# Kernel optimization log

Measured on AMD Instinct MI355X. Metric: run time of the kernel, lower is better.

The kernel has to match this reference:

```python
import jax, jax.numpy as jnp
import numpy as np

N_NODES = 50000
N_EDGES = 640000
IN_DIM = 128
HID_DIM = 128


def setup_inputs() -> dict:
    key = jax.random.key(0)
    k1, k2, k3 = jax.random.split(key, 3)
    x = jax.random.normal(k1, (N_NODES, IN_DIM), dtype=jnp.float32)
    edge_index = jax.random.randint(k2, (2, N_EDGES), 0, N_NODES, dtype=jnp.int64)
    # GCNConv linear weight (glorot-ish scale) and bias
    W = jax.random.normal(k3, (IN_DIM, HID_DIM), dtype=jnp.float32) * (1.0 / np.sqrt(IN_DIM))
    b = jnp.zeros((HID_DIM,), dtype=jnp.float32)
    return {"x": x, "edge_index": edge_index, "W": W, "b": b}


def reference(x, edge_index, W, b):
    # PyG GCNConv: add self-loops, symmetric normalization deg^{-1/2} A deg^{-1/2},
    # linear transform, scatter-add aggregation, bias; then ReLU (SimpleGCN).
    N = x.shape[0]
    loops = jnp.arange(N, dtype=edge_index.dtype)
    src = jnp.concatenate([edge_index[0], loops])  # [E+N]
    dst = jnp.concatenate([edge_index[1], loops])  # [E+N]

    # degree of destination nodes (including self-loops)
    ones = jnp.ones(src.shape[0], dtype=x.dtype)
    deg = jax.ops.segment_sum(ones, dst, num_segments=N)  # [N]
    dinv = jnp.where(deg > 0, jax.lax.rsqrt(deg), 0.0)
    norm = dinv[src] * dinv[dst]  # [E+N]

    h = x @ W  # [N, H] dense GEMM first (PyG transforms before propagate)
    msg = h[src] * norm[:, None]  # gather + scale, [E+N, H]
    agg = jax.ops.segment_sum(msg, dst, num_segments=N)  # scatter-add, [N, H]
    return jax.nn.relu(agg + b)
```

## Files before the change

### kernel.cpp

```cpp
#include <hip/hip_runtime.h>
#include <cstdint>

#define NN 50000
#define NE 640000
#define DIM 128
#define CAP 64
#define CSTRIDE 16
#define GEMM_TILES ((NN + 63) / 64)
#define FILL_BLOCKS (NE / 256)
#define GATHER_BLOCKS (NN * 16 / 256)

typedef __attribute__((ext_vector_type(8))) short bf16x8;
typedef __attribute__((ext_vector_type(8))) unsigned short u16x8;
typedef __attribute__((ext_vector_type(4))) float f32x4;

static __device__ __forceinline__ short f2bf(float f) {
    union { float f; uint32_t u; } v; v.f = f;
    uint32_t r = v.u + 0x7FFFu + ((v.u >> 16) & 1u);
    return (short)(r >> 16);
}
static __device__ __forceinline__ float bf2f(unsigned short u) {
    union { uint32_t u; float f; } v; v.u = ((uint32_t)u) << 16;
    return v.f;
}

__global__ __launch_bounds__(256) void k_gemm(const float* __restrict__ x,
                                              const float* __restrict__ W,
                                              unsigned short* __restrict__ h_bf,
                                              int4* __restrict__ cntp4) {
    __shared__ bf16x8 Bs[2048];
    const int tid = threadIdx.x;
    const int gid = blockIdx.x * 256 + tid;
    for (int i = gid; i < NN * CSTRIDE / 4; i += GEMM_TILES * 256)
        cntp4[i] = make_int4(0, 0, 0, 0);

    #pragma unroll
    for (int i = 0; i < 8; ++i) {
        const int t = tid + i * 256;
        const int n = t >> 8;
        const int kk = (t >> 6) & 3;
        const int l = t & 63;
        const int c = n * 16 + (l & 15);
        const int k0 = kk * 32 + (l >> 4) * 8;
        bf16x8 v;
        #pragma unroll
        for (int j = 0; j < 8; ++j) v[j] = f2bf(W[(k0 + j) * DIM + c]);
        Bs[t] = v;
    }

    const int wave = tid >> 6;
    const int lane = tid & 63;
    const int rbase = blockIdx.x * 64 + wave * 16;
    const int rA = rbase + (lane & 15);
    const int kg = lane >> 4;

    bf16x8 a[4];
    if (rA < NN) {
        const float* xr = x + (size_t)rA * DIM + kg * 8;
        #pragma unroll
        for (int kk = 0; kk < 4; ++kk) {
            const float4 f0 = *reinterpret_cast<const float4*>(xr + kk * 32);
            const float4 f1 = *reinterpret_cast<const float4*>(xr + kk * 32 + 4);
            a[kk][0] = f2bf(f0.x); a[kk][1] = f2bf(f0.y);
            a[kk][2] = f2bf(f0.z); a[kk][3] = f2bf(f0.w);
            a[kk][4] = f2bf(f1.x); a[kk][5] = f2bf(f1.y);
            a[kk][6] = f2bf(f1.z); a[kk][7] = f2bf(f1.w);
        }
    } else {
        #pragma unroll
        for (int kk = 0; kk < 4; ++kk) a[kk] = (bf16x8)0;
    }
    __syncthreads();

    const int rC0 = rbase + (lane >> 4) * 4;
    const int col = lane & 15;
    #pragma unroll
    for (int n = 0; n < 8; ++n) {
        f32x4 acc = {0.f, 0.f, 0.f, 0.f};
        #pragma unroll
        for (int kk = 0; kk < 4; ++kk) {
            const bf16x8 b = Bs[(n * 4 + kk) * 64 + lane];
            acc = __builtin_amdgcn_mfma_f32_16x16x32_bf16(a[kk], b, acc, 0, 0, 0);
        }
        #pragma unroll
        for (int i = 0; i < 4; ++i) {
            const int r = rC0 + i;
            if (r < NN)
                h_bf[(size_t)r * DIM + n * 16 + col] = (unsigned short)f2bf(acc[i]);
        }
    }
}

__global__ __launch_bounds__(256) void k_fill(const int* __restrict__ src,
                                              const int* __restrict__ dst,
                                              int* __restrict__ cntp,
                                              int* __restrict__ srt) {
    const int i = blockIdx.x * 256 + threadIdx.x;
    const int s = src[i];
    const int d = dst[i];
    const int pos = atomicAdd(&cntp[d * CSTRIDE], 1);
    srt[((size_t)d << 6) + pos] = s;
}

__global__ __launch_bounds__(256) void k_gather(const int* __restrict__ cntp,
                                                const int* __restrict__ srt,
                                                const unsigned short* __restrict__ h_bf,
                                                const float* __restrict__ bias,
                                                float* __restrict__ out) {
    const int t = blockIdx.x * 256 + threadIdx.x;
    const int n = t >> 4;
    if (n >= NN) return;
    const int lane = t & 15;
    const u16x8* __restrict__ h8 = reinterpret_cast<const u16x8*>(h_bf);

    const int deg = cntp[n * CSTRIDE];
    const float did = rsqrtf((float)deg + 1.0f);

    float acc[8];
    {
        const u16x8 hv = h8[(size_t)n * 16 + lane];
        #pragma unroll
        for (int j = 0; j < 8; ++j) acc[j] = bf2f(hv[j]) * did;
    }

    const int* __restrict__ bucket = srt + ((size_t)n << 6);
    int p = 0;
    for (; p + 3 < deg; p += 4) {
        const int s0 = bucket[p],     s1 = bucket[p + 1];
        const int s2 = bucket[p + 2], s3 = bucket[p + 3];
        const float n0 = rsqrtf((float)cntp[s0 * CSTRIDE] + 1.0f);
        const float n1 = rsqrtf((float)cntp[s1 * CSTRIDE] + 1.0f);
        const float n2 = rsqrtf((float)cntp[s2 * CSTRIDE] + 1.0f);
        const float n3 = rsqrtf((float)cntp[s3 * CSTRIDE] + 1.0f);
        const u16x8 v0 = h8[(size_t)s0 * 16 + lane];
        const u16x8 v1 = h8[(size_t)s1 * 16 + lane];
        const u16x8 v2 = h8[(size_t)s2 * 16 + lane];
        const u16x8 v3 = h8[(size_t)s3 * 16 + lane];
        #pragma unroll
        for (int j = 0; j < 8; ++j) acc[j] = fmaf(bf2f(v0[j]), n0, acc[j]);
        #pragma unroll
        for (int j = 0; j < 8; ++j) acc[j] = fmaf(bf2f(v1[j]), n1, acc[j]);
        #pragma unroll
        for (int j = 0; j < 8; ++j) acc[j] = fmaf(bf2f(v2[j]), n2, acc[j]);
        #pragma unroll
        for (int j = 0; j < 8; ++j) acc[j] = fmaf(bf2f(v3[j]), n3, acc[j]);
    }
    for (; p < deg; ++p) {
        const int s0 = bucket[p];
        const float n0 = rsqrtf((float)cntp[s0 * CSTRIDE] + 1.0f);
        const u16x8 v0 = h8[(size_t)s0 * 16 + lane];
        #pragma unroll
        for (int j = 0; j < 8; ++j) acc[j] = fmaf(bf2f(v0[j]), n0, acc[j]);
    }

    const float4 bv0 = reinterpret_cast<const float4*>(bias)[lane * 2];
    const float4 bv1 = reinterpret_cast<const float4*>(bias)[lane * 2 + 1];
    float4 o0, o1;
    o0.x = fmaxf(fmaf(did, acc[0], bv0.x), 0.f);
    o0.y = fmaxf(fmaf(did, acc[1], bv0.y), 0.f);
    o0.z = fmaxf(fmaf(did, acc[2], bv0.z), 0.f);
    o0.w = fmaxf(fmaf(did, acc[3], bv0.w), 0.f);
    o1.x = fmaxf(fmaf(did, acc[4], bv1.x), 0.f);
    o1.y = fmaxf(fmaf(did, acc[5], bv1.y), 0.f);
    o1.z = fmaxf(fmaf(did, acc[6], bv1.z), 0.f);
    o1.w = fmaxf(fmaf(did, acc[7], bv1.w), 0.f);
    float4* orow = reinterpret_cast<float4*>(out + (size_t)n * DIM) + lane * 2;
    orow[0] = o0;
    orow[1] = o1;
}

extern "C" void kernel_launch(void* const* d_in, const int* in_sizes, int n_in,
                              void* d_out, int out_size, void* d_ws, size_t ws_size,
                              hipStream_t stream) {
    const float* x  = (const float*)d_in[0];
    const int*   ei = (const int*)d_in[1];
    const float* W  = (const float*)d_in[2];
    const float* b  = (const float*)d_in[3];
    float* out = (float*)d_out;

    const int* src = ei;
    const int* dst = ei + NE;

    unsigned short* h_bf = (unsigned short*)d_ws;
    int* cntp = (int*)(h_bf + (size_t)NN * DIM);
    int* srt  = cntp + (size_t)NN * CSTRIDE;

    k_gemm<<<GEMM_TILES, 256, 0, stream>>>(x, W, h_bf, (int4*)cntp);
    k_fill<<<FILL_BLOCKS, 256, 0, stream>>>(src, dst, cntp, srt);
    k_gather<<<GATHER_BLOCKS, 256, 0, stream>>>(cntp, srt, h_bf, b, out);
}
```

Baseline: 93.29 us.

## Pack bf16 conversions, shrink counter stride, pair edges in fill, unroll gather by 8

GEMM operand conversion now uses a packed two-value float-to-bf16 intrinsic instead of manual per-element rounding. The degree counter stride drops from 16 ints to 4, which shrinks the zeroing work and the footprint of the scattered degree lookups. Each fill thread now handles two edges through int2 loads. The gather loop adds an 8-way unrolled path to keep more independent row loads in flight. Risks are more atomic contention from denser counters and higher register pressure in the gather kernel.

```diff
diff --git a/kernel.cpp b/kernel.cpp
--- a/kernel.cpp
+++ b/kernel.cpp
@@ -1,19 +1,28 @@
 #include <hip/hip_runtime.h>
+#include <hip/hip_bf16.h>
 #include <cstdint>
 
 #define NN 50000
 #define NE 640000
 #define DIM 128
 #define CAP 64
-#define CSTRIDE 16
+#define CSTRIDE 4
 #define GEMM_TILES ((NN + 63) / 64)
-#define FILL_BLOCKS (NE / 256)
+#define FILL_BLOCKS (NE / 2 / 256)
 #define GATHER_BLOCKS (NN * 16 / 256)
 
 typedef __attribute__((ext_vector_type(8))) short bf16x8;
 typedef __attribute__((ext_vector_type(8))) unsigned short u16x8;
 typedef __attribute__((ext_vector_type(4))) float f32x4;
 
+union bfpack { bf16x8 v; uint32_t u[4]; };
+
+static __device__ __forceinline__ uint32_t pk2bf(float lo, float hi) {
+    __hip_bfloat162 t = __float22bfloat162_rn(make_float2(lo, hi));
+    union { __hip_bfloat162 b; uint32_t u; } v;
+    v.b = t;
+    return v.u;
+}
 static __device__ __forceinline__ short f2bf(float f) {
     union { float f; uint32_t u; } v; v.f = f;
     uint32_t r = v.u + 0x7FFFu + ((v.u >> 16) & 1u);
@@ -42,10 +51,12 @@
         const int l = t & 63;
         const int c = n * 16 + (l & 15);
         const int k0 = kk * 32 + (l >> 4) * 8;
-        bf16x8 v;
-        #pragma unroll
-        for (int j = 0; j < 8; ++j) v[j] = f2bf(W[(k0 + j) * DIM + c]);
-        Bs[t] = v;
+        const float* wc = W + (size_t)k0 * DIM + c;
+        bfpack t8;
+        #pragma unroll
+        for (int j = 0; j < 4; ++j)
+            t8.u[j] = pk2bf(wc[(2 * j) * DIM], wc[(2 * j + 1) * DIM]);
+        Bs[t] = t8.v;
     }
 
     const int wave = tid >> 6;
@@ -61,10 +72,12 @@
         for (int kk = 0; kk < 4; ++kk) {
             const float4 f0 = *reinterpret_cast<const float4*>(xr + kk * 32);
             const float4 f1 = *reinterpret_cast<const float4*>(xr + kk * 32 + 4);
-            a[kk][0] = f2bf(f0.x); a[kk][1] = f2bf(f0.y);
-            a[kk][2] = f2bf(f0.z); a[kk][3] = f2bf(f0.w);
-            a[kk][4] = f2bf(f1.x); a[kk][5] = f2bf(f1.y);
-            a[kk][6] = f2bf(f1.z); a[kk][7] = f2bf(f1.w);
+            bfpack t8;
+            t8.u[0] = pk2bf(f0.x, f0.y);
+            t8.u[1] = pk2bf(f0.z, f0.w);
+            t8.u[2] = pk2bf(f1.x, f1.y);
+            t8.u[3] = pk2bf(f1.z, f1.w);
+            a[kk] = t8.v;
         }
     } else {
         #pragma unroll
@@ -91,15 +104,15 @@
     }
 }
 
-__global__ __launch_bounds__(256) void k_fill(const int* __restrict__ src,
-                                              const int* __restrict__ dst,
+__global__ __launch_bounds__(256) void k_fill(const int2* __restrict__ src2,
+                                              const int2* __restrict__ dst2,
                                               int* __restrict__ cntp,
                                               int* __restrict__ srt) {
     const int i = blockIdx.x * 256 + threadIdx.x;
-    const int s = src[i];
-    const int d = dst[i];
-    const int pos = atomicAdd(&cntp[d * CSTRIDE], 1);
-    srt[((size_t)d << 6) + pos] = s;
+    const int2 s = src2[i];
+    const int2 d = dst2[i];
+    srt[((size_t)d.x << 6) + atomicAdd(&cntp[d.x * CSTRIDE], 1)] = s.x;
+    srt[((size_t)d.y << 6) + atomicAdd(&cntp[d.y * CSTRIDE], 1)] = s.y;
 }
 
 __global__ __launch_bounds__(256) void k_gather(const int* __restrict__ cntp,
@@ -125,25 +138,35 @@
 
     const int* __restrict__ bucket = srt + ((size_t)n << 6);
     int p = 0;
+    for (; p + 7 < deg; p += 8) {
+        int s[8];
+        #pragma unroll
+        for (int q = 0; q < 8; ++q) s[q] = bucket[p + q];
+        float nw[8];
+        #pragma unroll
+        for (int q = 0; q < 8; ++q) nw[q] = rsqrtf((float)cntp[s[q] * CSTRIDE] + 1.0f);
+        u16x8 v[8];
+        #pragma unroll
+        for (int q = 0; q < 8; ++q) v[q] = h8[(size_t)s[q] * 16 + lane];
+        #pragma unroll
+        for (int q = 0; q < 8; ++q)
+            #pragma unroll
+            for (int j = 0; j < 8; ++j) acc[j] = fmaf(bf2f(v[q][j]), nw[q], acc[j]);
+    }
     for (; p + 3 < deg; p += 4) {
-        const int s0 = bucket[p],     s1 = bucket[p + 1];
-        const int s2 = bucket[p + 2], s3 = bucket[p + 3];
-        const float n0 = rsqrtf((float)cntp[s0 * CSTRIDE] + 1.0f);
-        const float n1 = rsqrtf((float)cntp[s1 * CSTRIDE] + 1.0f);
-        const float n2 = rsqrtf((float)cntp[s2 * CSTRIDE] + 1.0f);
-        const float n3 = rsqrtf((float)cntp[s3 * CSTRIDE] + 1.0f);
-        const u16x8 v0 = h8[(size_t)s0 * 16 + lane];
-        const u16x8 v1 = h8[(size_t)s1 * 16 + lane];
-        const u16x8 v2 = h8[(size_t)s2 * 16 + lane];
-        const u16x8 v3 = h8[(size_t)s3 * 16 + lane];
-        #pragma unroll
-        for (int j = 0; j < 8; ++j) acc[j] = fmaf(bf2f(v0[j]), n0, acc[j]);
-        #pragma unroll
-        for (int j = 0; j < 8; ++j) acc[j] = fmaf(bf2f(v1[j]), n1, acc[j]);
-        #pragma unroll
-        for (int j = 0; j < 8; ++j) acc[j] = fmaf(bf2f(v2[j]), n2, acc[j]);
-        #pragma unroll
-        for (int j = 0; j < 8; ++j) acc[j] = fmaf(bf2f(v3[j]), n3, acc[j]);
+        int s[4];
+        #pragma unroll
+        for (int q = 0; q < 4; ++q) s[q] = bucket[p + q];
+        float nw[4];
+        #pragma unroll
+        for (int q = 0; q < 4; ++q) nw[q] = rsqrtf((float)cntp[s[q] * CSTRIDE] + 1.0f);
+        u16x8 v[4];
+        #pragma unroll
+        for (int q = 0; q < 4; ++q) v[q] = h8[(size_t)s[q] * 16 + lane];
+        #pragma unroll
+        for (int q = 0; q < 4; ++q)
+            #pragma unroll
+            for (int j = 0; j < 8; ++j) acc[j] = fmaf(bf2f(v[q][j]), nw[q], acc[j]);
     }
     for (; p < deg; ++p) {
         const int s0 = bucket[p];
@@ -186,6 +209,7 @@
     int* srt  = cntp + (size_t)NN * CSTRIDE;
 
     k_gemm<<<GEMM_TILES, 256, 0, stream>>>(x, W, h_bf, (int4*)cntp);
-    k_fill<<<FILL_BLOCKS, 256, 0, stream>>>(src, dst, cntp, srt);
+    k_fill<<<FILL_BLOCKS, 256, 0, stream>>>((const int2*)src, (const int2*)dst,
+                                            cntp, srt);
     k_gather<<<GATHER_BLOCKS, 256, 0, stream>>>(cntp, srt, h_bf, b, out);
 }
```

Measured after the change: 83.85 us. 1.11x faster.
